# Kernel tuning notes

Hardware: AMD Instinct MI355X
Metric: run time of the kernel (lower is better)

## Reference

```python
import jax, jax.numpy as jnp
import numpy as np

BLOCK_SIZE = 32
STRIDE = 16
DIM = 128


def setup_inputs() -> dict:
    key = jax.random.key(0)
    ks = jax.random.split(key, 6)
    B, N, C = 8, 16384, DIM
    x = jax.random.normal(ks[0], (B, N, C), dtype=jnp.float32)
    pos = jax.random.normal(ks[1], (1, BLOCK_SIZE, C), dtype=jnp.float32) * 0.02
    # torch Linear stores W:(out,in); we store transposed (in,out) for x @ W
    fan_in1 = C * BLOCK_SIZE
    W1 = jax.random.uniform(ks[2], (fan_in1, 2 * C), dtype=jnp.float32,
                            minval=-1.0, maxval=1.0) / jnp.sqrt(fan_in1)
    b1 = jax.random.uniform(ks[3], (2 * C,), dtype=jnp.float32,
                            minval=-1.0, maxval=1.0) / jnp.sqrt(fan_in1)
    fan_in2 = 2 * C
    W2 = jax.random.uniform(ks[4], (fan_in2, C), dtype=jnp.float32,
                            minval=-1.0, maxval=1.0) / jnp.sqrt(fan_in2)
    b2 = jax.random.uniform(ks[5], (C,), dtype=jnp.float32,
                            minval=-1.0, maxval=1.0) / jnp.sqrt(fan_in2)
    return {"x": x, "pos": pos, "W1": W1, "b1": b1, "W2": W2, "b2": b2}


def reference(x, pos, W1, b1, W2, b2):
    B, N, C = x.shape
    l, d = BLOCK_SIZE, STRIDE
    if N < l:  # static shapes -> plain Python branch is fine
        return jnp.mean(x, axis=1, keepdims=True)
    num_blocks = (N - l) // d + 1
    # overlapping sliding-window gather: (nb, l) token indices
    idx = jnp.arange(num_blocks)[:, None] * d + jnp.arange(l)[None, :]
    blocks = x[:, idx, :] + pos[None]            # (B, nb, l, C)
    blocks = blocks.reshape(B, num_blocks, l * C)  # (B, nb, l*C)
    h = jax.nn.gelu(blocks @ W1 + b1, approximate=False)  # exact erf GELU (torch default)
    return h @ W2 + b2                           # (B, nb, C)
```

## Files before the change

### kernel.cpp

```cpp
#include <hip/hip_runtime.h>
#include <hip/hip_bf16.h>
#include <math.h>


typedef __attribute__((ext_vector_type(8))) short short8;
typedef __attribute__((ext_vector_type(4))) float f4;

#define OFF_BT   0u
#define OFF_W2T  (2u << 20)
#define OFF_PART ((2u << 20) + (64u << 10))
#define OFF_BIAS ((2u << 20) + (128u << 10))
#define OFF_P    (4u << 20)

static __device__ __forceinline__ unsigned short f2bf(float f) {
  union { float f; unsigned u; } v; v.f = f;
  return (unsigned short)((v.u + 0x7FFFu + ((v.u >> 16) & 1u)) >> 16);
}
static __device__ __forceinline__ float bf2f(unsigned short h) {
  union { unsigned u; float f; } v; v.u = ((unsigned)h) << 16;
  return v.f;
}
static __device__ __forceinline__ void gload_lds16(const void* g, void* l) {
  __builtin_amdgcn_global_load_lds(
      (const __attribute__((address_space(1))) void*)g,
      (__attribute__((address_space(3))) void*)l, 16, 0, 0);
}

__global__ __launch_bounds__(256) void k_prep(const float* __restrict__ W1,
                                              const float* __restrict__ pos,
                                              const float* __restrict__ W2,
                                              unsigned short* __restrict__ Bt,
                                              unsigned short* __restrict__ W2t,
                                              float* __restrict__ part) {
  __shared__ float T[64][65];
  const int w = blockIdx.x;
  const int t = threadIdx.x;
  if (w >= 256) {
    const int n = w - 256;
    W2t[n * 256 + t] = f2bf(W2[t * 128 + n]);
    return;
  }
  const int h = w >> 7, rem = w & 127, kt = rem >> 2, nt = rem & 3;
  const int krow0 = h * 2048 + kt * 64, col0 = nt * 64;
  const int lr = t >> 2, lc = (t & 3) * 16;
  const float* src = W1 + (size_t)(krow0 + lr) * 256 + col0 + lc;
#pragma unroll
  for (int i = 0; i < 4; ++i) {
    f4 v = *(const f4*)(src + i * 4);
#pragma unroll
    for (int q = 0; q < 4; ++q) T[lr][lc + i * 4 + q] = v[q];
  }
  __syncthreads();
  if (t < 64) {
    float s = 0.f;
#pragma unroll 8
    for (int k = 0; k < 64; ++k) s += T[k][t] * pos[krow0 + k];
    part[(h * 32 + kt) * 256 + col0 + t] = s;
  }
  const int nl = t >> 2, kc = (t & 3) * 16;
  short8 o0, o1;
#pragma unroll
  for (int i = 0; i < 8; ++i) o0[i] = (short)f2bf(T[kc + i][nl]);
#pragma unroll
  for (int i = 0; i < 8; ++i) o1[i] = (short)f2bf(T[kc + 8 + i][nl]);
  unsigned short* dst = Bt + (size_t)(256 * h + col0 + nl) * 2048 + kt * 64 + kc;
  *(short8*)dst = o0;
  *(short8*)(dst + 8) = o1;
}

__global__ __launch_bounds__(256) void k_bias(const float* __restrict__ b1,
                                              const float* __restrict__ part,
                                              float* __restrict__ bias) {
  int n = threadIdx.x;
  float s = b1[n];
#pragma unroll 8
  for (int g = 0; g < 64; ++g) s += part[g * 256 + n];
  bias[n] = s;
}

__global__ __launch_bounds__(256, 2) void k_gemm(const float* __restrict__ X,
                                                 const unsigned short* __restrict__ Bt,
                                                 unsigned short* __restrict__ P) {
  __shared__ __align__(16) char ldsbuf[3][24576];
  const int orig = blockIdx.x;
  const int wg = (orig & 7) * 128 + (orig >> 3);
  const int mt = wg >> 4;
  const int nt = (wg >> 2) & 3;
  const int ks_split = wg & 3;
  const int m0 = mt * 128, n0 = nt * 128;
  const int k0 = ks_split * 512;
  const int t = threadIdx.x;
  const int wid = t >> 6, lane = t & 63;
  const int wm = (wid >> 1) * 64, wn = (wid & 1) * 64;

  f4 acc[4][4];
#pragma unroll
  for (int i = 0; i < 4; ++i)
#pragma unroll
    for (int j = 0; j < 4; ++j) acc[i][j] = f4{0.f, 0.f, 0.f, 0.f};

#define ISSUE(BUF, KT)                                                     \
  do {                                                                     \
    const int kbase = k0 + (KT) * 32;                                      \
    _Pragma("unroll") for (int ii = 0; ii < 4; ++ii) {                     \
      const int row = wid * 32 + ii * 8 + (lane >> 3);                     \
      const int g = (lane & 7) ^ (row & 7);                                \
      const float* srcA = X + (size_t)(m0 + row) * 2048 + kbase + g * 4;   \
      gload_lds16(srcA, &ldsbuf[BUF][wid * 4096 + ii * 1024]);             \
    }                                                                      \
    _Pragma("unroll") for (int ii = 0; ii < 2; ++ii) {                     \
      const int rowb = ii * 64 + wid * 16 + (lane >> 2);                   \
      const int gb = (lane & 3) ^ (rowb & 3);                              \
      const unsigned short* srcB =                                         \
          Bt + (size_t)(n0 + rowb) * 2048 + kbase + gb * 8;                \
      gload_lds16(srcB, &ldsbuf[BUF][16384 + ii * 4096 + wid * 1024]);     \
    }                                                                      \
  } while (0)

#define COMPUTE(BUF)                                                       \
  do {                                                                     \
    const float* Ab = (const float*)&ldsbuf[BUF][0];                       \
    const unsigned short* Bb = (const unsigned short*)&ldsbuf[BUF][16384]; \
    short8 af[4], bfv[4];                                                  \
    _Pragma("unroll") for (int f = 0; f < 4; ++f) {                        \
      const int rowA = wm + f * 16 + (lane & 15);                          \
      const int c0 = (lane >> 4) * 2;                                      \
      f4 lo = *(const f4*)(Ab + rowA * 32 + ((c0 ^ (rowA & 7)) << 2));     \
      f4 hi = *(const f4*)(Ab + rowA * 32 + (((c0 + 1) ^ (rowA & 7)) << 2));\
      union { short8 s; unsigned u[4]; } pkv;                              \
      asm("v_cvt_pk_bf16_f32 %0, %1, %2" : "=v"(pkv.u[0])                  \
          : "v"(lo[0]), "v"(lo[1]));                                       \
      asm("v_cvt_pk_bf16_f32 %0, %1, %2" : "=v"(pkv.u[1])                  \
          : "v"(lo[2]), "v"(lo[3]));                                       \
      asm("v_cvt_pk_bf16_f32 %0, %1, %2" : "=v"(pkv.u[2])                  \
          : "v"(hi[0]), "v"(hi[1]));                                       \
      asm("v_cvt_pk_bf16_f32 %0, %1, %2" : "=v"(pkv.u[3])                  \
          : "v"(hi[2]), "v"(hi[3]));                                       \
      af[f] = pkv.s;                                                       \
      const int rowB = wn + f * 16 + (lane & 15);                          \
      const int cB = lane >> 4;                                            \
      bfv[f] = *(const short8*)(Bb + rowB * 32 + ((cB ^ (rowB & 3)) << 3));\
    }                                                                      \
    __builtin_amdgcn_s_setprio(1);                                         \
    _Pragma("unroll") for (int i2 = 0; i2 < 4; ++i2)                       \
        _Pragma("unroll") for (int j2 = 0; j2 < 4; ++j2)                   \
        acc[i2][j2] = __builtin_amdgcn_mfma_f32_16x16x32_bf16(             \
            af[i2], bfv[j2], acc[i2][j2], 0, 0, 0);                        \
    __builtin_amdgcn_s_setprio(0);                                         \
  } while (0)

  ISSUE(0, 0);
  ISSUE(1, 1);
  ISSUE(2, 2);
  __builtin_amdgcn_sched_barrier(0);
  asm volatile("s_waitcnt vmcnt(12)" ::: "memory");
  __builtin_amdgcn_s_barrier();
  __builtin_amdgcn_sched_barrier(0);

#pragma unroll
  for (int kt = 0; kt < 16; ++kt) {
    COMPUTE(kt % 3);
    __builtin_amdgcn_s_barrier();
    __builtin_amdgcn_sched_barrier(0);
    if (kt + 3 < 16) ISSUE(kt % 3, kt + 3);
    if (kt < 15) {
      __builtin_amdgcn_sched_barrier(0);
      if (kt < 13)       asm volatile("s_waitcnt vmcnt(12)" ::: "memory");
      else if (kt == 13) asm volatile("s_waitcnt vmcnt(6)" ::: "memory");
      else               asm volatile("s_waitcnt vmcnt(0)" ::: "memory");
      __builtin_amdgcn_s_barrier();
      __builtin_amdgcn_sched_barrier(0);
    }
  }
#undef ISSUE
#undef COMPUTE

  unsigned short* Pp = P + (size_t)ks_split * (8192 * 512);
  const int mb = m0 + wm, nb = n0 + wn;
#pragma unroll
  for (int i = 0; i < 4; ++i)
#pragma unroll
    for (int j = 0; j < 4; ++j) {
      const int row0 = mb + i * 16 + ((lane >> 4) << 2);
      const int col = nb + j * 16 + (lane & 15);
#pragma unroll
      for (int r = 0; r < 4; ++r)
        Pp[(size_t)(row0 + r) * 512 + col] = f2bf(acc[i][j][r]);
    }
}

__global__ __launch_bounds__(256) void k_comb(const unsigned short* __restrict__ P,
                                              const unsigned short* __restrict__ W2t,
                                              const float* __restrict__ bias,
                                              const float* __restrict__ b2,
                                              float* __restrict__ out) {
  __shared__ unsigned short W2s[128 * 256];
  __shared__ unsigned short Hs[32 * 256];
  const int wg = blockIdx.x;
  const int b = wg >> 5, jt = wg & 31;
  const int j0 = jt * 32;
  const int t = threadIdx.x;

  {
    const int row = t >> 1, halfc = (t & 1) * 128;
    const unsigned short* src = W2t + row * 256 + halfc;
    const int cbw = halfc >> 3;
#pragma unroll
    for (int i = 0; i < 16; ++i) {
      short8 v = *(const short8*)(src + i * 8);
      const int c = (cbw + i) ^ (row & 7);
      *(short8*)&W2s[row * 256 + c * 8] = v;
    }
  }
  {
    const int r = t >> 3, seg = t & 7;
    const int j = j0 + r;
    const size_t m = (size_t)b * 1024 + j;
    const size_t mp1 = (j < 1023) ? m + 1 : m;
    const float* bs = bias + seg * 32;
    const int cbh = seg * 4;
#pragma unroll
    for (int i = 0; i < 4; ++i) {
      float f0[8];
#pragma unroll
      for (int q = 0; q < 8; ++q) f0[q] = bs[i * 8 + q];
#pragma unroll
      for (int ksp = 0; ksp < 4; ++ksp) {
        const unsigned short* Pk = P + (size_t)ksp * (8192 * 512);
        short8 v0 = *(const short8*)(Pk + m * 512 + seg * 32 + i * 8);
        short8 v1 = *(const short8*)(Pk + mp1 * 512 + 256 + seg * 32 + i * 8);
#pragma unroll
        for (int q = 0; q < 8; ++q)
          f0[q] += bf2f((unsigned short)v0[q]) + bf2f((unsigned short)v1[q]);
      }
      short8 pk;
#pragma unroll
      for (int q = 0; q < 8; ++q) {
        float g = 0.5f * f0[q] * (1.f + erff(f0[q] * 0.70710678118f));
        pk[q] = (short)f2bf(g);
      }
      const int c = (cbh + i) ^ (r & 7);
      *(short8*)&Hs[r * 256 + c * 8] = pk;
    }
  }
  __syncthreads();

  const int wid = t >> 6, lane = t & 63;
  f4 acc[2][2];
#pragma unroll
  for (int i = 0; i < 2; ++i)
#pragma unroll
    for (int j = 0; j < 2; ++j) acc[i][j] = f4{0.f, 0.f, 0.f, 0.f};

#pragma unroll
  for (int ks = 0; ks < 8; ++ks) {
    short8 af[2], bfr[2];
    const int cc = ks * 4 + (lane >> 4);
#pragma unroll
    for (int f = 0; f < 2; ++f) {
      const int ra = f * 16 + (lane & 15);
      af[f] = *(const short8*)&Hs[ra * 256 + ((cc ^ (ra & 7)) << 3)];
      const int rb = wid * 32 + f * 16 + (lane & 15);
      bfr[f] = *(const short8*)&W2s[rb * 256 + ((cc ^ (rb & 7)) << 3)];
    }
#pragma unroll
    for (int i = 0; i < 2; ++i)
#pragma unroll
      for (int j = 0; j < 2; ++j)
        acc[i][j] = __builtin_amdgcn_mfma_f32_16x16x32_bf16(af[i], bfr[j],
                                                            acc[i][j], 0, 0, 0);
  }
#pragma unroll
  for (int i = 0; i < 2; ++i)
#pragma unroll
    for (int j = 0; j < 2; ++j) {
      const int row0 = i * 16 + ((lane >> 4) << 2);
      const int col = wid * 32 + j * 16 + (lane & 15);
      const float bb = b2[col];
#pragma unroll
      for (int r = 0; r < 4; ++r) {
        const int jj = j0 + row0 + r;
        if (jj < 1023)
          out[((size_t)b * 1023 + jj) * 128 + col] = acc[i][j][r] + bb;
      }
    }
}

extern "C" void kernel_launch(void* const* d_in, const int* in_sizes, int n_in,
                              void* d_out, int out_size, void* d_ws, size_t ws_size,
                              hipStream_t stream) {
  const float* x   = (const float*)d_in[0];
  const float* pos = (const float*)d_in[1];
  const float* W1  = (const float*)d_in[2];
  const float* b1  = (const float*)d_in[3];
  const float* W2  = (const float*)d_in[4];
  const float* b2  = (const float*)d_in[5];
  float* out = (float*)d_out;
  char* ws = (char*)d_ws;
  unsigned short* Bt  = (unsigned short*)(ws + OFF_BT);
  unsigned short* W2t = (unsigned short*)(ws + OFF_W2T);
  float* part         = (float*)(ws + OFF_PART);
  float* bias         = (float*)(ws + OFF_BIAS);
  unsigned short* P   = (unsigned short*)(ws + OFF_P);

  k_prep<<<384, 256, 0, stream>>>(W1, pos, W2, Bt, W2t, part);
  k_bias<<<1, 256, 0, stream>>>(b1, part, bias);
  k_gemm<<<1024, 256, 0, stream>>>(x, Bt, P);
  k_comb<<<256, 256, 0, stream>>>(P, W2t, bias, b2, out);
}
```

Before: 59.93 us.

## Pre-convert X to bf16 in a separate kernel and shrink GEMM LDS tiles

Adds a kernel that converts the whole fp32 input X to bf16 in workspace before the GEMM. The GEMM then streams bf16 A tiles, which halves A-tile LDS and global traffic per tile and removes the in-loop fp32-to-bf16 conversion. The smaller LDS footprint allows raising launch bounds to three blocks per CU. The cost is an extra full pass over X: 64 MB read and 32 MB written.

```diff
diff --git a/kernel.cpp b/kernel.cpp
--- a/kernel.cpp
+++ b/kernel.cpp
@@ -11,6 +11,7 @@
 #define OFF_PART ((2u << 20) + (64u << 10))
 #define OFF_BIAS ((2u << 20) + (128u << 10))
 #define OFF_P    (4u << 20)
+#define OFF_XB   (36u << 20)
 
 static __device__ __forceinline__ unsigned short f2bf(float f) {
   union { float f; unsigned u; } v; v.f = f;
@@ -24,6 +25,24 @@
   __builtin_amdgcn_global_load_lds(
       (const __attribute__((address_space(1))) void*)g,
       (__attribute__((address_space(3))) void*)l, 16, 0, 0);
+}
+
+__global__ __launch_bounds__(256) void k_xcvt(const float* __restrict__ X,
+                                              unsigned short* __restrict__ Xb) {
+  const size_t t = (size_t)blockIdx.x * 256 + threadIdx.x;
+  const float* src = X + t * 32;
+  unsigned short* dst = Xb + t * 32;
+#pragma unroll
+  for (int i = 0; i < 4; ++i) {
+    f4 a = *(const f4*)(src + i * 8);
+    f4 b = *(const f4*)(src + i * 8 + 4);
+    union { short8 s; unsigned u[4]; } pk;
+    asm("v_cvt_pk_bf16_f32 %0, %1, %2" : "=v"(pk.u[0]) : "v"(a[0]), "v"(a[1]));
+    asm("v_cvt_pk_bf16_f32 %0, %1, %2" : "=v"(pk.u[1]) : "v"(a[2]), "v"(a[3]));
+    asm("v_cvt_pk_bf16_f32 %0, %1, %2" : "=v"(pk.u[2]) : "v"(b[0]), "v"(b[1]));
+    asm("v_cvt_pk_bf16_f32 %0, %1, %2" : "=v"(pk.u[3]) : "v"(b[2]), "v"(b[3]));
+    *(short8*)(dst + i * 8) = pk.s;
+  }
 }
 
 __global__ __launch_bounds__(256) void k_prep(const float* __restrict__ W1,
@@ -78,10 +97,10 @@
   bias[n] = s;
 }
 
-__global__ __launch_bounds__(256, 2) void k_gemm(const float* __restrict__ X,
+__global__ __launch_bounds__(256, 3) void k_gemm(const unsigned short* __restrict__ Xb,
                                                  const unsigned short* __restrict__ Bt,
                                                  unsigned short* __restrict__ P) {
-  __shared__ __align__(16) char ldsbuf[3][24576];
+  __shared__ __align__(16) char lds[3][16384];
   const int orig = blockIdx.x;
   const int wg = (orig & 7) * 128 + (orig >> 3);
   const int mt = wg >> 4;
@@ -102,44 +121,31 @@
 #define ISSUE(BUF, KT)                                                     \
   do {                                                                     \
     const int kbase = k0 + (KT) * 32;                                      \
-    _Pragma("unroll") for (int ii = 0; ii < 4; ++ii) {                     \
-      const int row = wid * 32 + ii * 8 + (lane >> 3);                     \
-      const int g = (lane & 7) ^ (row & 7);                                \
-      const float* srcA = X + (size_t)(m0 + row) * 2048 + kbase + g * 4;   \
-      gload_lds16(srcA, &ldsbuf[BUF][wid * 4096 + ii * 1024]);             \
-    }                                                                      \
     _Pragma("unroll") for (int ii = 0; ii < 2; ++ii) {                     \
-      const int rowb = ii * 64 + wid * 16 + (lane >> 2);                   \
-      const int gb = (lane & 3) ^ (rowb & 3);                              \
+      const int row = ii * 64 + wid * 16 + (lane >> 2);                    \
+      const int ch = (lane & 3) ^ ((row >> 1) & 3);                        \
+      const unsigned short* srcA =                                         \
+          Xb + (size_t)(m0 + row) * 2048 + kbase + ch * 8;                 \
+      gload_lds16(srcA, &lds[BUF][ii * 4096 + wid * 1024]);                \
       const unsigned short* srcB =                                         \
-          Bt + (size_t)(n0 + rowb) * 2048 + kbase + gb * 8;                \
-      gload_lds16(srcB, &ldsbuf[BUF][16384 + ii * 4096 + wid * 1024]);     \
+          Bt + (size_t)(n0 + row) * 2048 + kbase + ch * 8;                 \
+      gload_lds16(srcB, &lds[BUF][8192 + ii * 4096 + wid * 1024]);         \
     }                                                                      \
   } while (0)
 
 #define COMPUTE(BUF)                                                       \
   do {                                                                     \
-    const float* Ab = (const float*)&ldsbuf[BUF][0];                       \
-    const unsigned short* Bb = (const unsigned short*)&ldsbuf[BUF][16384]; \
+    const unsigned short* Ab = (const unsigned short*)&lds[BUF][0];        \
+    const unsigned short* Bb = (const unsigned short*)&lds[BUF][8192];     \
     short8 af[4], bfv[4];                                                  \
+    const int cA = lane >> 4;                                              \
     _Pragma("unroll") for (int f = 0; f < 4; ++f) {                        \
       const int rowA = wm + f * 16 + (lane & 15);                          \
-      const int c0 = (lane >> 4) * 2;                                      \
-      f4 lo = *(const f4*)(Ab + rowA * 32 + ((c0 ^ (rowA & 7)) << 2));     \
-      f4 hi = *(const f4*)(Ab + rowA * 32 + (((c0 + 1) ^ (rowA & 7)) << 2));\
-      union { short8 s; unsigned u[4]; } pkv;                              \
-      asm("v_cvt_pk_bf16_f32 %0, %1, %2" : "=v"(pkv.u[0])                  \
-          : "v"(lo[0]), "v"(lo[1]));                                       \
-      asm("v_cvt_pk_bf16_f32 %0, %1, %2" : "=v"(pkv.u[1])                  \
-          : "v"(lo[2]), "v"(lo[3]));                                       \
-      asm("v_cvt_pk_bf16_f32 %0, %1, %2" : "=v"(pkv.u[2])                  \
-          : "v"(hi[0]), "v"(hi[1]));                                       \
-      asm("v_cvt_pk_bf16_f32 %0, %1, %2" : "=v"(pkv.u[3])                  \
-          : "v"(hi[2]), "v"(hi[3]));                                       \
-      af[f] = pkv.s;                                                       \
+      af[f] = *(const short8*)(Ab + rowA * 32 +                            \
+                               ((cA ^ ((rowA >> 1) & 3)) << 3));           \
       const int rowB = wn + f * 16 + (lane & 15);                          \
-      const int cB = lane >> 4;                                            \
-      bfv[f] = *(const short8*)(Bb + rowB * 32 + ((cB ^ (rowB & 3)) << 3));\
+      bfv[f] = *(const short8*)(Bb + rowB * 32 +                           \
+                                ((cA ^ ((rowB >> 1) & 3)) << 3));          \
     }                                                                      \
     __builtin_amdgcn_s_setprio(1);                                         \
     _Pragma("unroll") for (int i2 = 0; i2 < 4; ++i2)                       \
@@ -153,7 +159,7 @@
   ISSUE(1, 1);
   ISSUE(2, 2);
   __builtin_amdgcn_sched_barrier(0);
-  asm volatile("s_waitcnt vmcnt(12)" ::: "memory");
+  asm volatile("s_waitcnt vmcnt(8)" ::: "memory");
   __builtin_amdgcn_s_barrier();
   __builtin_amdgcn_sched_barrier(0);
 
@@ -165,8 +171,8 @@
     if (kt + 3 < 16) ISSUE(kt % 3, kt + 3);
     if (kt < 15) {
       __builtin_amdgcn_sched_barrier(0);
-      if (kt < 13)       asm volatile("s_waitcnt vmcnt(12)" ::: "memory");
-      else if (kt == 13) asm volatile("s_waitcnt vmcnt(6)" ::: "memory");
+      if (kt < 13)       asm volatile("s_waitcnt vmcnt(8)" ::: "memory");
+      else if (kt == 13) asm volatile("s_waitcnt vmcnt(4)" ::: "memory");
       else               asm volatile("s_waitcnt vmcnt(0)" ::: "memory");
       __builtin_amdgcn_s_barrier();
       __builtin_amdgcn_sched_barrier(0);
@@ -302,9 +308,11 @@
   float* part         = (float*)(ws + OFF_PART);
   float* bias         = (float*)(ws + OFF_BIAS);
   unsigned short* P   = (unsigned short*)(ws + OFF_P);
-
+  unsigned short* Xb  = (unsigned short*)(ws + OFF_XB);
+
+  k_xcvt<<<2048, 256, 0, stream>>>(x, Xb);
   k_prep<<<384, 256, 0, stream>>>(W1, pos, W2, Bt, W2t, part);
   k_bias<<<1, 256, 0, stream>>>(b1, part, bias);
-  k_gemm<<<1024, 256, 0, stream>>>(x, Bt, P);
+  k_gemm<<<1024, 256, 0, stream>>>(Xb, Bt, P);
   k_comb<<<256, 256, 0, stream>>>(P, W2t, bias, b2, out);
 }
```

Result: slower. 69.57 us (+16.1%).

## Drop split-K in main GEMM, use 512-thread workgroups with double-buffered K=64 tiles

Applied to the files above, without the earlier changes.

The main GEMM no longer splits K four ways. Each of 256 workgroups of 512 threads now computes a full-K 128x128 output tile, using double-buffered 64-wide K slices with a new LDS swizzle. This removes the four partial-sum bf16 writes and the four-way reads and reduction in the combine kernel, which now reads a single partial buffer. In exchange there are only 256 workgroups, which may underfill the GPU, and each workgroup runs a longer serial K loop.

```diff
diff --git a/kernel.cpp b/kernel.cpp
--- a/kernel.cpp
+++ b/kernel.cpp
@@ -78,114 +78,120 @@
   bias[n] = s;
 }
 
-__global__ __launch_bounds__(256, 2) void k_gemm(const float* __restrict__ X,
+__global__ __launch_bounds__(512, 2) void k_gemm(const float* __restrict__ X,
                                                  const unsigned short* __restrict__ Bt,
                                                  unsigned short* __restrict__ P) {
-  __shared__ __align__(16) char ldsbuf[3][24576];
+  __shared__ __align__(16) char lds[2][49152];
   const int orig = blockIdx.x;
-  const int wg = (orig & 7) * 128 + (orig >> 3);
-  const int mt = wg >> 4;
-  const int nt = (wg >> 2) & 3;
-  const int ks_split = wg & 3;
+  const int wgid = (orig & 7) * 32 + (orig >> 3);
+  const int mt = wgid >> 2, nt = wgid & 3;
   const int m0 = mt * 128, n0 = nt * 128;
-  const int k0 = ks_split * 512;
   const int t = threadIdx.x;
   const int wid = t >> 6, lane = t & 63;
-  const int wm = (wid >> 1) * 64, wn = (wid & 1) * 64;
-
-  f4 acc[4][4];
-#pragma unroll
-  for (int i = 0; i < 4; ++i)
-#pragma unroll
-    for (int j = 0; j < 4; ++j) acc[i][j] = f4{0.f, 0.f, 0.f, 0.f};
+  const int wr = wid >> 1, wc = wid & 1;
+
+  f4 acc[2][4];
+#pragma unroll
+  for (int m = 0; m < 2; ++m)
+#pragma unroll
+    for (int n = 0; n < 4; ++n) acc[m][n] = f4{0.f, 0.f, 0.f, 0.f};
 
 #define ISSUE(BUF, KT)                                                     \
   do {                                                                     \
-    const int kbase = k0 + (KT) * 32;                                      \
+    const int kf = (KT) * 64;                                              \
     _Pragma("unroll") for (int ii = 0; ii < 4; ++ii) {                     \
-      const int row = wid * 32 + ii * 8 + (lane >> 3);                     \
-      const int g = (lane & 7) ^ (row & 7);                                \
-      const float* srcA = X + (size_t)(m0 + row) * 2048 + kbase + g * 4;   \
-      gload_lds16(srcA, &ldsbuf[BUF][wid * 4096 + ii * 1024]);             \
+      const int s = ii * 512 + t;                                          \
+      const int row = s >> 4, c16 = s & 15;                                \
+      const int e = ((row & 7) << 1) | ((row >> 3) & 1);                   \
+      gload_lds16(X + (size_t)(m0 + row) * 2048 + kf + ((c16 ^ e) << 2),   \
+                  &lds[BUF][ii * 8192 + wid * 1024]);                      \
     }                                                                      \
     _Pragma("unroll") for (int ii = 0; ii < 2; ++ii) {                     \
-      const int rowb = ii * 64 + wid * 16 + (lane >> 2);                   \
-      const int gb = (lane & 3) ^ (rowb & 3);                              \
-      const unsigned short* srcB =                                         \
-          Bt + (size_t)(n0 + rowb) * 2048 + kbase + gb * 8;                \
-      gload_lds16(srcB, &ldsbuf[BUF][16384 + ii * 4096 + wid * 1024]);     \
+      const int s = ii * 512 + t;                                          \
+      const int row = s >> 3, c8 = s & 7;                                  \
+      gload_lds16(Bt + (size_t)(n0 + row) * 2048 + kf +                    \
+                      ((c8 ^ (row & 7)) << 3),                             \
+                  &lds[BUF][32768 + ii * 8192 + wid * 1024]);              \
     }                                                                      \
   } while (0)
 
 #define COMPUTE(BUF)                                                       \
   do {                                                                     \
-    const float* Ab = (const float*)&ldsbuf[BUF][0];                       \
-    const unsigned short* Bb = (const unsigned short*)&ldsbuf[BUF][16384]; \
-    short8 af[4], bfv[4];                                                  \
-    _Pragma("unroll") for (int f = 0; f < 4; ++f) {                        \
-      const int rowA = wm + f * 16 + (lane & 15);                          \
-      const int c0 = (lane >> 4) * 2;                                      \
-      f4 lo = *(const f4*)(Ab + rowA * 32 + ((c0 ^ (rowA & 7)) << 2));     \
-      f4 hi = *(const f4*)(Ab + rowA * 32 + (((c0 + 1) ^ (rowA & 7)) << 2));\
-      union { short8 s; unsigned u[4]; } pkv;                              \
-      asm("v_cvt_pk_bf16_f32 %0, %1, %2" : "=v"(pkv.u[0])                  \
-          : "v"(lo[0]), "v"(lo[1]));                                       \
-      asm("v_cvt_pk_bf16_f32 %0, %1, %2" : "=v"(pkv.u[1])                  \
-          : "v"(lo[2]), "v"(lo[3]));                                       \
-      asm("v_cvt_pk_bf16_f32 %0, %1, %2" : "=v"(pkv.u[2])                  \
-          : "v"(hi[0]), "v"(hi[1]));                                       \
-      asm("v_cvt_pk_bf16_f32 %0, %1, %2" : "=v"(pkv.u[3])                  \
-          : "v"(hi[2]), "v"(hi[3]));                                       \
-      af[f] = pkv.s;                                                       \
-      const int rowB = wn + f * 16 + (lane & 15);                          \
-      const int cB = lane >> 4;                                            \
-      bfv[f] = *(const short8*)(Bb + rowB * 32 + ((cB ^ (rowB & 3)) << 3));\
+    const float* Ab = (const float*)&lds[BUF][0];                          \
+    const unsigned short* Bb = (const unsigned short*)&lds[BUF][32768];    \
+    _Pragma("unroll") for (int ks = 0; ks < 2; ++ks) {                     \
+      short8 af[2];                                                        \
+      short8 bfv[4];                                                       \
+      _Pragma("unroll") for (int m = 0; m < 2; ++m) {                      \
+        const int row = wr * 32 + m * 16 + (lane & 15);                    \
+        const int e = ((row & 7) << 1) | ((row >> 3) & 1);                 \
+        const int cp = ks * 8 + (lane >> 4) * 2;                           \
+        f4 lo = *(const f4*)(Ab + row * 64 + ((cp ^ e) << 2));             \
+        f4 hi = *(const f4*)(Ab + row * 64 + (((cp + 1) ^ e) << 2));       \
+        union { short8 s8; unsigned u[4]; } pk;                            \
+        asm("v_cvt_pk_bf16_f32 %0, %1, %2" : "=v"(pk.u[0])                 \
+            : "v"(lo[0]), "v"(lo[1]));                                     \
+        asm("v_cvt_pk_bf16_f32 %0, %1, %2" : "=v"(pk.u[1])                 \
+            : "v"(lo[2]), "v"(lo[3]));                                     \
+        asm("v_cvt_pk_bf16_f32 %0, %1, %2" : "=v"(pk.u[2])                 \
+            : "v"(hi[0]), "v"(hi[1]));                                     \
+        asm("v_cvt_pk_bf16_f32 %0, %1, %2" : "=v"(pk.u[3])                 \
+            : "v"(hi[2]), "v"(hi[3]));                                     \
+        af[m] = pk.s8;                                                     \
+      }                                                                    \
+      _Pragma("unroll") for (int n = 0; n < 4; ++n) {                      \
+        const int row = wc * 64 + n * 16 + (lane & 15);                    \
+        const int ch = ks * 4 + (lane >> 4);                               \
+        bfv[n] = *(const short8*)(Bb + row * 64 +                          \
+                                  ((ch ^ (row & 7)) << 3));                \
+      }                                                                    \
+      __builtin_amdgcn_s_setprio(1);                                       \
+      _Pragma("unroll") for (int m = 0; m < 2; ++m)                        \
+        _Pragma("unroll") for (int n = 0; n < 4; ++n)                      \
+          acc[m][n] = __builtin_amdgcn_mfma_f32_16x16x32_bf16(             \
+              af[m], bfv[n], acc[m][n], 0, 0, 0);                          \
+      __builtin_amdgcn_s_setprio(0);                                       \
     }                                                                      \
-    __builtin_amdgcn_s_setprio(1);                                         \
-    _Pragma("unroll") for (int i2 = 0; i2 < 4; ++i2)                       \
-        _Pragma("unroll") for (int j2 = 0; j2 < 4; ++j2)                   \
-        acc[i2][j2] = __builtin_amdgcn_mfma_f32_16x16x32_bf16(             \
-            af[i2], bfv[j2], acc[i2][j2], 0, 0, 0);                        \
-    __builtin_amdgcn_s_setprio(0);                                         \
   } while (0)
 
   ISSUE(0, 0);
   ISSUE(1, 1);
-  ISSUE(2, 2);
   __builtin_amdgcn_sched_barrier(0);
-  asm volatile("s_waitcnt vmcnt(12)" ::: "memory");
+  asm volatile("s_waitcnt vmcnt(6)" ::: "memory");
   __builtin_amdgcn_s_barrier();
   __builtin_amdgcn_sched_barrier(0);
 
-#pragma unroll
-  for (int kt = 0; kt < 16; ++kt) {
-    COMPUTE(kt % 3);
+#pragma unroll 2
+  for (int kt = 0; kt < 32; ++kt) {
+    COMPUTE(kt & 1);
+    __builtin_amdgcn_sched_barrier(0);
     __builtin_amdgcn_s_barrier();
     __builtin_amdgcn_sched_barrier(0);
-    if (kt + 3 < 16) ISSUE(kt % 3, kt + 3);
-    if (kt < 15) {
+    if (kt < 30) {
+      ISSUE(kt & 1, kt + 2);
       __builtin_amdgcn_sched_barrier(0);
-      if (kt < 13)       asm volatile("s_waitcnt vmcnt(12)" ::: "memory");
-      else if (kt == 13) asm volatile("s_waitcnt vmcnt(6)" ::: "memory");
-      else               asm volatile("s_waitcnt vmcnt(0)" ::: "memory");
+      asm volatile("s_waitcnt vmcnt(6)" ::: "memory");
       __builtin_amdgcn_s_barrier();
       __builtin_amdgcn_sched_barrier(0);
+    } else if (kt == 30) {
+      asm volatile("s_waitcnt vmcnt(0)" ::: "memory");
+      __builtin_amdgcn_s_barrier();
+      __builtin_amdgcn_sched_barrier(0);
     }
   }
 #undef ISSUE
 #undef COMPUTE
 
-  unsigned short* Pp = P + (size_t)ks_split * (8192 * 512);
-  const int mb = m0 + wm, nb = n0 + wn;
-#pragma unroll
-  for (int i = 0; i < 4; ++i)
-#pragma unroll
-    for (int j = 0; j < 4; ++j) {
-      const int row0 = mb + i * 16 + ((lane >> 4) << 2);
-      const int col = nb + j * 16 + (lane & 15);
+  const int mb = m0 + wr * 32, nb = n0 + wc * 64;
+#pragma unroll
+  for (int m = 0; m < 2; ++m)
+#pragma unroll
+    for (int n = 0; n < 4; ++n) {
+      const int row0 = mb + m * 16 + ((lane >> 4) << 2);
+      const int col = nb + n * 16 + (lane & 15);
 #pragma unroll
       for (int r = 0; r < 4; ++r)
-        Pp[(size_t)(row0 + r) * 512 + col] = f2bf(acc[i][j][r]);
+        P[(size_t)(row0 + r) * 512 + col] = f2bf(acc[m][n][r]);
     }
 }
 
@@ -217,26 +223,20 @@
     const int j = j0 + r;
     const size_t m = (size_t)b * 1024 + j;
     const size_t mp1 = (j < 1023) ? m + 1 : m;
+    const unsigned short* p0 = P + m * 512 + seg * 32;
+    const unsigned short* p1 = P + mp1 * 512 + 256 + seg * 32;
     const float* bs = bias + seg * 32;
     const int cbh = seg * 4;
 #pragma unroll
     for (int i = 0; i < 4; ++i) {
-      float f0[8];
-#pragma unroll
-      for (int q = 0; q < 8; ++q) f0[q] = bs[i * 8 + q];
-#pragma unroll
-      for (int ksp = 0; ksp < 4; ++ksp) {
-        const unsigned short* Pk = P + (size_t)ksp * (8192 * 512);
-        short8 v0 = *(const short8*)(Pk + m * 512 + seg * 32 + i * 8);
-        short8 v1 = *(const short8*)(Pk + mp1 * 512 + 256 + seg * 32 + i * 8);
-#pragma unroll
-        for (int q = 0; q < 8; ++q)
-          f0[q] += bf2f((unsigned short)v0[q]) + bf2f((unsigned short)v1[q]);
-      }
+      short8 v0 = *(const short8*)(p0 + i * 8);
+      short8 v1 = *(const short8*)(p1 + i * 8);
       short8 pk;
 #pragma unroll
       for (int q = 0; q < 8; ++q) {
-        float g = 0.5f * f0[q] * (1.f + erff(f0[q] * 0.70710678118f));
+        float f = bf2f((unsigned short)v0[q]) + bf2f((unsigned short)v1[q]) +
+                  bs[i * 8 + q];
+        float g = 0.5f * f * (1.f + erff(f * 0.70710678118f));
         pk[q] = (short)f2bf(g);
       }
       const int c = (cbh + i) ^ (r & 7);
@@ -305,6 +305,6 @@
 
   k_prep<<<384, 256, 0, stream>>>(W1, pos, W2, Bt, W2t, part);
   k_bias<<<1, 256, 0, stream>>>(b1, part, bias);
-  k_gemm<<<1024, 256, 0, stream>>>(x, Bt, P);
+  k_gemm<<<256, 512, 0, stream>>>(x, Bt, P);
   k_comb<<<256, 256, 0, stream>>>(P, W2t, bias, b2, out);
 }
```

Measured after the change: 53.91 us. -10.0%, faster.
